# Optimization experiments

Hardware: AMD Instinct MI355X
Metric: run time of the kernel (lower is better)

## Reference

```python
import jax, jax.numpy as jnp
import numpy as np

ALPHA = 0.2  # LeakyReLU negative slope
EPS = 1e-6


def gam(x):
    # relu6(x+3)/3 + eps
    return jnp.clip(x + 3.0, 0.0, 6.0) / 3.0 + EPS


def leaky(x):
    return jnp.where(x >= 0, x, ALPHA * x)


def relu_bt(x):
    # threshold at detached inf-norm of input: min(leaky_relu(x), ||x||_inf)
    t = jax.lax.stop_gradient(jnp.max(jnp.abs(x)))
    return jnp.minimum(leaky(x), t)


def setup_inputs() -> dict:
    key = jax.random.key(0)
    ks = jax.random.split(key, 8)
    N, E, Din, Dout = 100000, 1600000, 256, 64
    return {
        "input": jax.random.normal(ks[0], (N, Din), dtype=jnp.float32),
        "edge": jax.random.randint(ks[1], (2, E), 0, N, dtype=jnp.int32),
        "W_high": jax.random.normal(ks[2], (Din, Dout), dtype=jnp.float32) * 0.06,
        "W_low": jax.random.normal(ks[3], (Din, Dout), dtype=jnp.float32) * 0.06,
        "a_high": jax.random.normal(ks[4], (1, 4 * Dout), dtype=jnp.float32) * 0.09,
        "a_low": jax.random.normal(ks[5], (1, 4 * Dout), dtype=jnp.float32) * 0.09,
        "c_high": jax.random.uniform(ks[6], (1, 1), dtype=jnp.float32),
        "c_low": jax.random.uniform(ks[7], (1, 1), dtype=jnp.float32),
    }


def reference(input, edge, W_high, W_low, a_high, a_low, c_high, c_low):
    N = input.shape[0]
    F = W_high.shape[1]
    src, dst = edge[0], edge[1]

    theta_high = gam(c_high) / 2.0  # [1,1]
    theta_low = gam(c_low) / 2.0

    h_high = relu_bt(input @ W_high)  # [N,F]
    h_low = relu_bt(input @ W_low)

    hh_s, hh_d = h_high[src], h_high[dst]  # [E,F]
    hl_s, hl_d = h_low[src], h_low[dst]

    ah = a_high[0]
    al = a_low[0]
    # a . [h_i, h_j, h_i+h_j, h_i-h_j] folded into per-endpoint coefficients
    # NOTE: original code uses h_high for the first two blocks of the LOW branch too.
    score_high = hh_s @ (ah[:F] + ah[2 * F:3 * F] + ah[3 * F:]) \
               + hh_d @ (ah[F:2 * F] + ah[2 * F:3 * F] - ah[3 * F:])  # [E]
    score_low = hh_s @ al[:F] + hh_d @ al[F:2 * F] \
              + hl_s @ (al[2 * F:3 * F] + al[3 * F:]) \
              + hl_d @ (al[2 * F:3 * F] - al[3 * F:])

    e_high = jnp.exp(-leaky(score_high / jnp.linalg.norm(a_high)))  # [E]
    e_low = jnp.exp(-leaky(score_low / jnp.linalg.norm(a_low)))

    # sparse COO spmm: rowsum and weighted aggregation
    rowsum_high = jax.ops.segment_sum(e_high, src, num_segments=N)[:, None]  # [N,1]
    rowsum_low = jax.ops.segment_sum(e_low, src, num_segments=N)[:, None]
    hp_high = jax.ops.segment_sum(e_high[:, None] * hh_d, src, num_segments=N)  # [N,F]
    hp_low = jax.ops.segment_sum(e_low[:, None] * hl_d, src, num_segments=N)

    hp_high = hp_high / (rowsum_high + theta_high)
    hp_low = hp_low / (rowsum_low + theta_low)

    # concat=True branch
    return relu_bt(jnp.concatenate([hp_high, hp_low], axis=1))  # [N,2F]
```

## Files before the change

kernel.cpp:

```cpp
#include <hip/hip_runtime.h>
#include <hip/hip_bf16.h>
#include <hip/hip_fp16.h>
#include <math.h>

typedef unsigned short ushort_t;
typedef unsigned int uint_t;
typedef __attribute__((ext_vector_type(8))) short short8;
typedef __attribute__((ext_vector_type(4))) float floatx4;
typedef __attribute__((ext_vector_type(4))) uint_t uintx4;
typedef __attribute__((ext_vector_type(4))) int intx4;

#define ALPHA 0.2f
#define CAP 64
#define NXCD 8

__device__ __forceinline__ float leaky(float x) { return x >= 0.0f ? x : ALPHA * x; }

__device__ __forceinline__ float bf2f(ushort_t u) {
    union { uint_t i; float f; } v; v.i = ((uint_t)u) << 16; return v.f;
}
__device__ __forceinline__ float bflo(uint_t p) {
    union { uint_t i; float f; } v; v.i = p << 16; return v.f;
}
__device__ __forceinline__ float bfhi(uint_t p) {
    union { uint_t i; float f; } v; v.i = p & 0xffff0000u; return v.f;
}
__device__ __forceinline__ ushort_t f2bf(float f) {
    union { float f; uint_t i; } v; v.f = f;
    return (ushort_t)((v.i + 0x8000u) >> 16);
}
__device__ __forceinline__ uint_t pack_bf2(float a, float b) {
    union { float f; uint_t i; } ua, ub; ua.f = a; ub.f = b;
    return ((ua.i + 0x8000u) >> 16) | ((ub.i + 0x8000u) & 0xffff0000u);
}

__global__ void prep_wtrans_kernel(const float* __restrict__ Wh, const float* __restrict__ Wl,
                                   ushort_t* __restrict__ WTg,
                                   const float* __restrict__ ah, const float* __restrict__ al,
                                   const float* __restrict__ ch, const float* __restrict__ cl,
                                   float* __restrict__ coef, float* __restrict__ consts) {
    int t = threadIdx.x;
    if (blockIdx.x < 128) {
        int c = blockIdx.x;
        float v = (c < 64) ? Wh[t * 64 + c] : Wl[t * 64 + (c - 64)];
        WTg[c * 256 + t] = f2bf(v);
        return;
    }
    __shared__ float red[256];
    float va = ah[t];
    red[t] = va * va;
    __syncthreads();
    for (int s = 128; s > 0; s >>= 1) { if (t < s) red[t] += red[t + s]; __syncthreads(); }
    float sum_h = red[0];
    __syncthreads();
    float vb = al[t];
    red[t] = vb * vb;
    __syncthreads();
    for (int s = 128; s > 0; s >>= 1) { if (t < s) red[t] += red[t + s]; __syncthreads(); }
    float sum_l = red[0];

    if (t == 0) {
        consts[0] = 1.0f / sqrtf(sum_h);
        consts[1] = 1.0f / sqrtf(sum_l);
        float c = ch[0];
        float g = fminf(fmaxf(c + 3.0f, 0.0f), 6.0f) / 3.0f + 1e-6f;
        consts[2] = g * 0.5f;
        c = cl[0];
        g = fminf(fmaxf(c + 3.0f, 0.0f), 6.0f) / 3.0f + 1e-6f;
        consts[3] = g * 0.5f;
    }
    if (t < 128) {
        int f = t;
        float c0, c1, c2, c3;
        if (f < 64) {
            c0 = ah[f] + ah[128 + f] + ah[192 + f];
            c1 = ah[64 + f] + ah[128 + f] - ah[192 + f];
            c2 = al[f];
            c3 = al[64 + f];
        } else {
            int g = f - 64;
            c0 = 0.0f;
            c1 = 0.0f;
            c2 = al[128 + g] + al[192 + g];
            c3 = al[128 + g] - al[192 + g];
        }
        coef[0 * 128 + f] = c0;
        coef[1 * 128 + f] = c1;
        coef[2 * 128 + f] = c2;
        coef[3 * 128 + f] = c3;
    }
}

__global__ __launch_bounds__(256, 4) void gemm_kernel(const float* __restrict__ in,
                                                      const ushort_t* __restrict__ WTg,
                                                      const float* __restrict__ coef,
                                                      ushort_t* __restrict__ hcat,
                                                      float* __restrict__ s4, int N) {
    __shared__ ushort_t WT[128 * 128];
    __shared__ float coefS[512];
    int tid = threadIdx.x;
    for (int i = tid; i < 512; i += 256) coefS[i] = coef[i];

    int wave = tid >> 6, lane = tid & 63;
    int quad = lane >> 4, m16 = lane & 15;
    int rowbase = blockIdx.x * 64 + wave * 16;
    int arow = rowbase + m16;
    if (arow >= N) arow = N - 1;

    floatx4 acc[8];
#pragma unroll
    for (int ct = 0; ct < 8; ++ct) acc[ct] = (floatx4){0.0f, 0.0f, 0.0f, 0.0f};

    const uint4* WTg4 = (const uint4*)WTg;

#pragma unroll
    for (int kh = 0; kh < 2; ++kh) {
        if (kh) __syncthreads();
        for (int i = tid; i < 2048; i += 256) {
            int c = i >> 4, j = i & 15;
            int sj = j ^ (c & 7);
            uint4 v = WTg4[c * 32 + kh * 16 + j];
            *(uint4*)&WT[c * 128 + sj * 8] = v;
        }
        __syncthreads();
#pragma unroll
        for (int ks = 0; ks < 4; ++ks) {
            const floatx4* ap = (const floatx4*)(in + (size_t)arow * 256 + kh * 128 + ks * 32 + quad * 8);
            floatx4 a0 = __builtin_nontemporal_load(ap);
            floatx4 a1 = __builtin_nontemporal_load(ap + 1);
            union { uintx4 u; short8 s; } av;
            av.u[0] = pack_bf2(a0[0], a0[1]);
            av.u[1] = pack_bf2(a0[2], a0[3]);
            av.u[2] = pack_bf2(a1[0], a1[1]);
            av.u[3] = pack_bf2(a1[2], a1[3]);
#pragma unroll
            for (int ct = 0; ct < 8; ++ct) {
                int c = ct * 16 + m16;
                int sch = (ks * 4 + quad) ^ (c & 7);
                short8 b = *(const short8*)&WT[c * 128 + sch * 8];
                acc[ct] = __builtin_amdgcn_mfma_f32_16x16x32_bf16(av.s, b, acc[ct], 0, 0, 0);
            }
        }
    }

    float hv[8][4];
#pragma unroll
    for (int ct = 0; ct < 8; ++ct) {
#pragma unroll
        for (int r = 0; r < 4; ++r) {
            int row = rowbase + quad * 4 + r;
            float v = leaky(acc[ct][r]);
            hv[ct][r] = v;
            if (row < N) hcat[(size_t)row * 128 + ct * 16 + m16] = f2bf(v);
        }
    }
#pragma unroll
    for (int r = 0; r < 4; ++r) {
        int row = rowbase + quad * 4 + r;
        float p0 = 0, p1 = 0, p2 = 0, p3 = 0;
#pragma unroll
        for (int ct = 0; ct < 8; ++ct) {
            int c = ct * 16 + m16;
            float h = hv[ct][r];
            p0 += coefS[c] * h;
            p1 += coefS[128 + c] * h;
            p2 += coefS[256 + c] * h;
            p3 += coefS[384 + c] * h;
        }
#pragma unroll
        for (int off = 1; off < 16; off <<= 1) {
            p0 += __shfl_xor(p0, off);
            p1 += __shfl_xor(p1, off);
            p2 += __shfl_xor(p2, off);
            p3 += __shfl_xor(p3, off);
        }
        if (m16 == 0 && row < N) {
            floatx4 v = {p0, p1, p2, p3};
            *(floatx4*)&s4[(size_t)row * 4] = v;
        }
    }
}

__global__ __launch_bounds__(256) void scatter_kernel(const int* __restrict__ edge,
                                                      int* __restrict__ cursor,
                                                      uint_t* __restrict__ elist,
                                                      int E, int N) {
    int xcd = blockIdx.x & (NXCD - 1);
    int chunk = blockIdx.x >> 3;
    int TN = (N + NXCD - 1) / NXCD;
    int lo = xcd * TN;
    int hiN = lo + TN;
    int base = chunk * 2048 + threadIdx.x * 8;

    int sv[8], dv[8];
    if (base + 8 <= E && (E & 3) == 0) {
        intx4 s0 = __builtin_nontemporal_load((const intx4*)(edge + base));
        intx4 s1 = __builtin_nontemporal_load((const intx4*)(edge + base + 4));
        intx4 d0 = __builtin_nontemporal_load((const intx4*)(edge + E + base));
        intx4 d1 = __builtin_nontemporal_load((const intx4*)(edge + E + base + 4));
#pragma unroll
        for (int j = 0; j < 4; ++j) { sv[j] = s0[j]; sv[4 + j] = s1[j]; dv[j] = d0[j]; dv[4 + j] = d1[j]; }
    } else {
#pragma unroll
        for (int j = 0; j < 8; ++j) {
            bool ok = base + j < E;
            sv[j] = ok ? edge[base + j] : -1;
            dv[j] = ok ? edge[E + base + j] : 0;
        }
    }

    bool m[8];
    int pos[8];
#pragma unroll
    for (int j = 0; j < 8; ++j) m[j] = (sv[j] >= lo) & (sv[j] < hiN);
#pragma unroll
    for (int j = 0; j < 8; ++j) {
        pos[j] = 0;
        if (m[j]) pos[j] = atomicAdd(&cursor[sv[j]], 1);
    }
#pragma unroll
    for (int j = 0; j < 8; ++j) {
        if (m[j] && pos[j] < CAP) elist[(size_t)sv[j] * CAP + pos[j]] = (uint_t)dv[j];
    }
}

__global__ __launch_bounds__(256) void aggregate_kernel(const int* __restrict__ deg,
                                                        const uint_t* __restrict__ elist,
                                                        const ushort_t* __restrict__ hcat,
                                                        const float* __restrict__ s4,
                                                        const float* __restrict__ consts,
                                                        float* __restrict__ out, int N) {
    int w = (blockIdx.x * blockDim.x + threadIdx.x) >> 6;
    int lane = threadIdx.x & 63;
    if (w >= N) return;
    int d = deg[w];
    if (d > CAP) d = CAP;

    float s_own_h = s4[(size_t)w * 4 + 0];
    float s_own_l = s4[(size_t)w * 4 + 2];
    float inv_h = consts[0], inv_l = consts[1];
    int dst = 0;
    float wh = 0.0f, wl = 0.0f;
    if (lane < d) {
        dst = (int)elist[(size_t)w * CAP + lane];
        float4 sv = *(const float4*)&s4[(size_t)dst * 4];
        wh = __expf(-leaky((s_own_h + sv.y) * inv_h));
        wl = __expf(-leaky((s_own_l + sv.w) * inv_l));
    }
    uint_t wp = (uint_t)__half_as_ushort(__float2half(wh))
              | ((uint_t)__half_as_ushort(__float2half(wl)) << 16);
    float rsh = wh, rsl = wl;
#pragma unroll
    for (int off = 1; off < 64; off <<= 1) {
        rsh += __shfl_xor(rsh, off);
        rsl += __shfl_xor(rsl, off);
    }

    bool hi = lane < 32;
    int wsh = hi ? 0 : 16;
    const ushort_t* hbase = hcat + lane * 2;

    float a0 = 0, a1 = 0, b0 = 0, b1 = 0;
    int j = 0;
    for (; j + 4 <= d; j += 4) {
        int d0 = __shfl(dst, j);
        int d1 = __shfl(dst, j + 1);
        int d2 = __shfl(dst, j + 2);
        int d3 = __shfl(dst, j + 3);
        uint_t u0 = (uint_t)__shfl((int)wp, j);
        uint_t u1 = (uint_t)__shfl((int)wp, j + 1);
        uint_t u2 = (uint_t)__shfl((int)wp, j + 2);
        uint_t u3 = (uint_t)__shfl((int)wp, j + 3);
        uint_t p0 = *(const uint_t*)&hbase[(size_t)d0 * 128];
        uint_t p1 = *(const uint_t*)&hbase[(size_t)d1 * 128];
        uint_t p2 = *(const uint_t*)&hbase[(size_t)d2 * 128];
        uint_t p3 = *(const uint_t*)&hbase[(size_t)d3 * 128];
        float w0 = __half2float(__ushort_as_half((ushort_t)(u0 >> wsh)));
        float w1 = __half2float(__ushort_as_half((ushort_t)(u1 >> wsh)));
        float w2 = __half2float(__ushort_as_half((ushort_t)(u2 >> wsh)));
        float w3 = __half2float(__ushort_as_half((ushort_t)(u3 >> wsh)));
        a0 += w0 * bflo(p0); a1 += w0 * bfhi(p0);
        b0 += w1 * bflo(p1); b1 += w1 * bfhi(p1);
        a0 += w2 * bflo(p2); a1 += w2 * bfhi(p2);
        b0 += w3 * bflo(p3); b1 += w3 * bfhi(p3);
    }
    for (; j < d; ++j) {
        int dj = __shfl(dst, j);
        uint_t uj = (uint_t)__shfl((int)wp, j);
        uint_t p = *(const uint_t*)&hbase[(size_t)dj * 128];
        float wt = __half2float(__ushort_as_half((ushort_t)(uj >> wsh)));
        a0 += wt * bflo(p);
        a1 += wt * bfhi(p);
    }

    float acc0 = a0 + b0;
    float acc1 = a1 + b1;
    float rsum = hi ? rsh : rsl;
    float theta = hi ? consts[2] : consts[3];
    float inv = 1.0f / (rsum + theta);
    float2 r;
    r.x = leaky(acc0 * inv);
    r.y = leaky(acc1 * inv);
    *(float2*)&out[(size_t)w * 128 + lane * 2] = r;
}

extern "C" void kernel_launch(void* const* d_in, const int* in_sizes, int n_in,
                              void* d_out, int out_size, void* d_ws, size_t ws_size,
                              hipStream_t stream) {
    const float* input = (const float*)d_in[0];
    const int* edge = (const int*)d_in[1];
    const float* Wh = (const float*)d_in[2];
    const float* Wl = (const float*)d_in[3];
    const float* ah = (const float*)d_in[4];
    const float* al = (const float*)d_in[5];
    const float* ch = (const float*)d_in[6];
    const float* cl = (const float*)d_in[7];
    int N = in_sizes[0] / 256;
    int E = in_sizes[1] / 2;
    float* out = (float*)d_out;

    char* ws = (char*)d_ws;
    size_t off = 0;
    uint_t* elist = (uint_t*)(ws + off);     off += (size_t)N * CAP * 4;
    ushort_t* hcat = (ushort_t*)(ws + off);  off += (size_t)N * 128 * 2;
    float* s4 = (float*)(ws + off);          off += (size_t)N * 4 * 4;
    int* cursor = (int*)(ws + off);          off += (size_t)N * 4;
    ushort_t* WTg = (ushort_t*)(ws + off);   off += 128 * 256 * 2;
    float* coef = (float*)(ws + off);        off += 4 * 128 * 4;
    float* consts = (float*)(ws + off);      off += 64;

    hipMemsetAsync(cursor, 0, (size_t)N * 4, stream);
    prep_wtrans_kernel<<<129, 256, 0, stream>>>(Wh, Wl, WTg, ah, al, ch, cl, coef, consts);
    gemm_kernel<<<(N + 63) / 64, 256, 0, stream>>>(input, WTg, coef, hcat, s4, N);
    int nchunks = (E + 2047) / 2048;
    scatter_kernel<<<nchunks * NXCD, 256, 0, stream>>>(edge, cursor, elist, E, N);
    aggregate_kernel<<<(N + 3) / 4, 256, 0, stream>>>(cursor, elist, hcat, s4, consts, out, N);
}
```

Baseline: 349.3 us.

## Pad per-node degree counters to 64B lines and unroll gather loop by eight

Each node's atomic degree counter now sits in its own 64-byte slot, so atomics to neighbouring nodes no longer contend on the same cache line. The memset grows to N*64 bytes to match. The aggregation gather loop is unrolled to eight edges with four accumulator pairs, giving more loads in flight. The edge loads in the scatter kernel drop the nontemporal hint and the E%4 alignment check. Costs are 16x more counter memory and memset traffic, scattered single-int degree reads, and possible misaligned vector loads if E is not a multiple of 4.

```diff
diff --git a/kernel.cpp b/kernel.cpp
--- a/kernel.cpp
+++ b/kernel.cpp
@@ -13,6 +13,7 @@
 #define ALPHA 0.2f
 #define CAP 64
 #define NXCD 8
+#define CPAD 16
 
 __device__ __forceinline__ float leaky(float x) { return x >= 0.0f ? x : ALPHA * x; }
 
@@ -193,11 +194,11 @@
     int base = chunk * 2048 + threadIdx.x * 8;
 
     int sv[8], dv[8];
-    if (base + 8 <= E && (E & 3) == 0) {
-        intx4 s0 = __builtin_nontemporal_load((const intx4*)(edge + base));
-        intx4 s1 = __builtin_nontemporal_load((const intx4*)(edge + base + 4));
-        intx4 d0 = __builtin_nontemporal_load((const intx4*)(edge + E + base));
-        intx4 d1 = __builtin_nontemporal_load((const intx4*)(edge + E + base + 4));
+    if (base + 8 <= E) {
+        intx4 s0 = *(const intx4*)(edge + base);
+        intx4 s1 = *(const intx4*)(edge + base + 4);
+        intx4 d0 = *(const intx4*)(edge + E + base);
+        intx4 d1 = *(const intx4*)(edge + E + base + 4);
 #pragma unroll
         for (int j = 0; j < 4; ++j) { sv[j] = s0[j]; sv[4 + j] = s1[j]; dv[j] = d0[j]; dv[4 + j] = d1[j]; }
     } else {
@@ -216,7 +217,7 @@
 #pragma unroll
     for (int j = 0; j < 8; ++j) {
         pos[j] = 0;
-        if (m[j]) pos[j] = atomicAdd(&cursor[sv[j]], 1);
+        if (m[j]) pos[j] = atomicAdd(&cursor[(size_t)sv[j] * CPAD], 1);
     }
 #pragma unroll
     for (int j = 0; j < 8; ++j) {
@@ -233,7 +234,7 @@
     int w = (blockIdx.x * blockDim.x + threadIdx.x) >> 6;
     int lane = threadIdx.x & 63;
     if (w >= N) return;
-    int d = deg[w];
+    int d = deg[(size_t)w * CPAD];
     if (d > CAP) d = CAP;
 
     float s_own_h = s4[(size_t)w * 4 + 0];
@@ -260,41 +261,40 @@
     int wsh = hi ? 0 : 16;
     const ushort_t* hbase = hcat + lane * 2;
 
-    float a0 = 0, a1 = 0, b0 = 0, b1 = 0;
+    float2 c0 = {0.f, 0.f}, c1 = {0.f, 0.f}, c2 = {0.f, 0.f}, c3 = {0.f, 0.f};
     int j = 0;
-    for (; j + 4 <= d; j += 4) {
-        int d0 = __shfl(dst, j);
-        int d1 = __shfl(dst, j + 1);
-        int d2 = __shfl(dst, j + 2);
-        int d3 = __shfl(dst, j + 3);
-        uint_t u0 = (uint_t)__shfl((int)wp, j);
-        uint_t u1 = (uint_t)__shfl((int)wp, j + 1);
-        uint_t u2 = (uint_t)__shfl((int)wp, j + 2);
-        uint_t u3 = (uint_t)__shfl((int)wp, j + 3);
-        uint_t p0 = *(const uint_t*)&hbase[(size_t)d0 * 128];
-        uint_t p1 = *(const uint_t*)&hbase[(size_t)d1 * 128];
-        uint_t p2 = *(const uint_t*)&hbase[(size_t)d2 * 128];
-        uint_t p3 = *(const uint_t*)&hbase[(size_t)d3 * 128];
-        float w0 = __half2float(__ushort_as_half((ushort_t)(u0 >> wsh)));
-        float w1 = __half2float(__ushort_as_half((ushort_t)(u1 >> wsh)));
-        float w2 = __half2float(__ushort_as_half((ushort_t)(u2 >> wsh)));
-        float w3 = __half2float(__ushort_as_half((ushort_t)(u3 >> wsh)));
-        a0 += w0 * bflo(p0); a1 += w0 * bfhi(p0);
-        b0 += w1 * bflo(p1); b1 += w1 * bfhi(p1);
-        a0 += w2 * bflo(p2); a1 += w2 * bfhi(p2);
-        b0 += w3 * bflo(p3); b1 += w3 * bfhi(p3);
+    for (; j + 8 <= d; j += 8) {
+        int dj[8];
+        uint_t uj[8];
+#pragma unroll
+        for (int k = 0; k < 8; ++k) {
+            dj[k] = __shfl(dst, j + k);
+            uj[k] = (uint_t)__shfl((int)wp, j + k);
+        }
+        uint_t pj[8];
+#pragma unroll
+        for (int k = 0; k < 8; ++k) pj[k] = *(const uint_t*)&hbase[(size_t)dj[k] * 128];
+#pragma unroll
+        for (int k = 0; k < 8; ++k) {
+            float wt = __half2float(__ushort_as_half((ushort_t)(uj[k] >> wsh)));
+            float lo0 = bflo(pj[k]), hi1 = bfhi(pj[k]);
+            if ((k & 3) == 0)      { c0.x += wt * lo0; c0.y += wt * hi1; }
+            else if ((k & 3) == 1) { c1.x += wt * lo0; c1.y += wt * hi1; }
+            else if ((k & 3) == 2) { c2.x += wt * lo0; c2.y += wt * hi1; }
+            else                   { c3.x += wt * lo0; c3.y += wt * hi1; }
+        }
     }
     for (; j < d; ++j) {
         int dj = __shfl(dst, j);
         uint_t uj = (uint_t)__shfl((int)wp, j);
         uint_t p = *(const uint_t*)&hbase[(size_t)dj * 128];
         float wt = __half2float(__ushort_as_half((ushort_t)(uj >> wsh)));
-        a0 += wt * bflo(p);
-        a1 += wt * bfhi(p);
-    }
-
-    float acc0 = a0 + b0;
-    float acc1 = a1 + b1;
+        c0.x += wt * bflo(p);
+        c0.y += wt * bfhi(p);
+    }
+
+    float acc0 = (c0.x + c1.x) + (c2.x + c3.x);
+    float acc1 = (c0.y + c1.y) + (c2.y + c3.y);
     float rsum = hi ? rsh : rsl;
     float theta = hi ? consts[2] : consts[3];
     float inv = 1.0f / (rsum + theta);
@@ -324,12 +324,12 @@
     uint_t* elist = (uint_t*)(ws + off);     off += (size_t)N * CAP * 4;
     ushort_t* hcat = (ushort_t*)(ws + off);  off += (size_t)N * 128 * 2;
     float* s4 = (float*)(ws + off);          off += (size_t)N * 4 * 4;
-    int* cursor = (int*)(ws + off);          off += (size_t)N * 4;
+    int* cursor = (int*)(ws + off);          off += (size_t)N * CPAD * 4;
     ushort_t* WTg = (ushort_t*)(ws + off);   off += 128 * 256 * 2;
     float* coef = (float*)(ws + off);        off += 4 * 128 * 4;
     float* consts = (float*)(ws + off);      off += 64;
 
-    hipMemsetAsync(cursor, 0, (size_t)N * 4, stream);
+    hipMemsetAsync(cursor, 0, (size_t)N * CPAD * 4, stream);
     prep_wtrans_kernel<<<129, 256, 0, stream>>>(Wh, Wl, WTg, ah, al, ch, cl, coef, consts);
     gemm_kernel<<<(N + 63) / 64, 256, 0, stream>>>(input, WTg, coef, hcat, s4, N);
     int nchunks = (E + 2047) / 2048;
```

New measurement: 347.7 us. About the same (-0.5%).
